# Optimization experiments

Measured on AMD Instinct MI355X. Metric: run time of the kernel, lower is better.

## Reference

```python
import jax, jax.numpy as jnp
import numpy as np
import math

B, T, E = 16, 4096, 1024
WIN = 15
EPS = 1e-6
HALF = T // 2


def _make_linear(key, out_f, in_f):
    k1, k2 = jax.random.split(key)
    lim = 1.0 / math.sqrt(in_f)
    W = jax.random.uniform(k1, (out_f, in_f), minval=-lim, maxval=lim, dtype=jnp.float32)
    b = jax.random.uniform(k2, (out_f,), minval=-lim, maxval=lim, dtype=jnp.float32)
    return W, b


def setup_inputs() -> dict:
    key = jax.random.key(0)
    ks = jax.random.split(key, 5)
    x = jax.random.normal(ks[0], (B, T, E), dtype=jnp.float32)
    taper = jnp.linspace(1.0, 0.0, T, dtype=jnp.float32)
    cW1, cb1 = _make_linear(ks[1], HALF, T)
    cW2, cb2 = _make_linear(ks[2], HALF, HALF)
    pW1, pb1 = _make_linear(ks[3], HALF, T)
    pW2, pb2 = _make_linear(ks[4], HALF, HALF)
    return {"x": x, "taper": taper,
            "cW1": cW1, "cb1": cb1, "cW2": cW2, "cb2": cb2,
            "pW1": pW1, "pb1": pb1, "pW2": pW2, "pb2": pb2}


def _compressor(h, W1, b1, W2, b2):
    # Linear -> SiLU -> Linear -> Tanh  (torch Linear: y = h @ W^T + b)
    h = jax.nn.silu(h @ W1.T + b1)
    return jnp.tanh(h @ W2.T + b2)


def _tdiff_raw(c0):
    Bb, Tt = c0.shape
    xp = jnp.pad(c0, ((0, 0), (WIN, 0)))  # left pad with zeros
    num = jnp.zeros_like(c0)
    for d in range(1, WIN + 1):  # small fixed loop over window lags
        num = num + float(d) * jax.lax.dynamic_slice_in_dim(xp, WIN - d, Tt, axis=1)
    i = jnp.arange(Tt, dtype=jnp.float32)
    s = jnp.minimum(i, float(WIN))
    norm = s * (s + 1.0) * 0.5
    return jnp.where(norm > 0, num / jnp.maximum(norm, 1.0), 0.0)


def reference(x, taper, cW1, cb1, cW2, cb2, pW1, pb1, pW2, pb2):
    x_t = x * taper[None, :, None]          # (B,T,E) tapered in time
    c0 = x_t[..., 0]                         # (B,T)
    r = jnp.abs(c0) + EPS
    start = jnp.where(c0 >= 0, 0.0, jnp.float32(math.pi))
    v = jnp.clip(x_t[..., 1:] / r[..., None], -1.0 + EPS, 1.0 - EPS)
    phases = start + jnp.arcsin(v).sum(axis=-1)  # (B,T)
    tdiff = _compressor(_tdiff_raw(c0), pW1, pb1, pW2, pb2)   # (B,T/2)
    thash = _compressor(phases, cW1, cb1, cW2, cb2)           # (B,T/2)
    return jnp.stack([thash, tdiff], axis=-1)                 # (B,T/2,2)
```

## Files before the change

### kernel.cpp

```cpp
#include <hip/hip_runtime.h>
#include <math.h>

#define BB 16
#define TT 4096
#define EE 1024
#define HALF 2048
#define WIN 15
#define EPSF 1e-6f
#define PI_F   3.14159265358979323846f
#define PIO2_F 1.57079632679489662f

__device__ __forceinline__ float asin_clamped(float t, float LO, float HI) {
    float c  = __builtin_amdgcn_fmed3f(t, LO, HI);
    float a  = fabsf(c);
    float z1 = c * c;
    float z2 = fmaf(a, -0.5f, 0.5f);
    bool big = a > 0.5f;
    float z  = big ? z2 : z1;
    float sq;
    asm("v_sqrt_f32 %0, %1" : "=v"(sq) : "v"(z2));
    float s  = big ? sq : a;
    float p = fmaf(z, 4.2163199048e-2f, 2.4181311049e-2f);
    p = fmaf(z, p, 4.5470025998e-2f);
    p = fmaf(z, p, 7.4953002686e-2f);
    p = fmaf(z, p, 1.6666752422e-1f);
    float r  = fmaf(s * z, p, s);
    float rb = fmaf(-2.0f, r, PIO2_F);
    r = big ? rb : r;
    return copysignf(r, c);
}

__global__ void phase_tdiff_kernel(const float* __restrict__ x,
                                   const float* __restrict__ taper,
                                   float* __restrict__ phases_b,
                                   float* __restrict__ tdiff_b) {
    const int wave = threadIdx.x >> 6;
    const int lane = threadIdx.x & 63;
    const int row  = blockIdx.x * 4 + wave;
    const int b = row >> 12;
    const int t = row & (TT - 1);
    const float tap = taper[t];
    const float* xr = x + (size_t)row * EE;

    float xd = 0.0f, tapd = 0.0f;
    const int td = t - lane;
    const bool do_d = (lane >= 1) && (lane <= WIN) && (lane <= t);
    if (do_d) {
        xd   = x[((size_t)b * TT + td) * EE];
        tapd = taper[td];
    }

    const float c0 = xr[0] * tap;
    const float r = fabsf(c0) + EPSF;
    const float scale = tap / r;
    const float start = (c0 >= 0.0f) ? 0.0f : PI_F;
    const float LO = -1.0f + EPSF, HI = 1.0f - EPSF;

    const float4* xr4 = (const float4*)xr;
    float sum = 0.0f;
    #pragma unroll
    for (int j = 0; j < 4; ++j) {
        float4 v = xr4[j * 64 + lane];
        float a0 = asin_clamped(v.x * scale, LO, HI);
        if ((j | lane) == 0) a0 = 0.0f;
        sum += a0;
        sum += asin_clamped(v.y * scale, LO, HI);
        sum += asin_clamped(v.z * scale, LO, HI);
        sum += asin_clamped(v.w * scale, LO, HI);
    }
    #pragma unroll
    for (int off = 32; off > 0; off >>= 1)
        sum += __shfl_xor(sum, off, 64);

    float contrib = do_d ? ((float)lane * xd * tapd) : 0.0f;
    #pragma unroll
    for (int off = 8; off > 0; off >>= 1)
        contrib += __shfl_xor(contrib, off, 64);

    if (lane == 0) {
        phases_b[b * TT + t] = start + sum;
        const int s = (t < WIN) ? t : WIN;
        const float norm = 0.5f * (float)s * (float)(s + 1);
        tdiff_b[b * TT + t] = (norm > 0.0f) ? (contrib / norm) : 0.0f;
    }
}

__device__ __forceinline__ void gld_lds16(const float* g, float* l) {
    __builtin_amdgcn_global_load_lds(
        (const __attribute__((address_space(1))) unsigned int*)g,
        (__attribute__((address_space(3))) unsigned int*)l,
        16, 0, 0);
}

template <int K, int MODE>
__global__ void __launch_bounds__(256)
gemm_kernel(const float* __restrict__ A0, const float* __restrict__ W0,
            const float* __restrict__ bias0, float* __restrict__ out0,
            const float* __restrict__ A1, const float* __restrict__ W1,
            const float* __restrict__ bias1, float* __restrict__ out1) {
    constexpr int KT = 512;
    constexpr int NT = K / KT;
    constexpr int LROW = KT + 4;
    __shared__ float als[2][16 * LROW];

    const int nb = HALF / 8;
    const int g = blockIdx.x / nb;
    const int obase = (blockIdx.x % nb) * 8;

    const float* A    = g ? A1 : A0;
    const float* W    = g ? W1 : W0;
    const float* bias = g ? bias1 : bias0;
    float* out        = g ? out1 : out0;

    const int wv   = threadIdx.x >> 6;
    const int lane = threadIdx.x & 63;
    const int col0 = obase + wv * 2;
    const int col1 = col0 + 1;
    const float* w0p = W + (size_t)col0 * K;
    const float* w1p = W + (size_t)col1 * K;

    auto stage = [&](int t, int s) {
        #pragma unroll
        for (int i = 0; i < 4; ++i) {
            const int br = wv * 4 + i;
            const float* src = A + (size_t)br * K + t * KT + lane * 4;
            float* dst = &als[s][br * LROW];
            gld_lds16(src, dst);
            gld_lds16(src + 256, dst + 256);
        }
    };

    float acc0[16], acc1[16];
    #pragma unroll
    for (int i = 0; i < 16; ++i) { acc0[i] = 0.0f; acc1[i] = 0.0f; }

    stage(0, 0);

    for (int t = 0; t < NT; ++t) {
        const int cur = t & 1;

        float4 w0v[2], w1v[2];
        #pragma unroll
        for (int s2 = 0; s2 < 2; ++s2) {
            w0v[s2] = *(const float4*)(w0p + t * KT + s2 * 256 + lane * 4);
            w1v[s2] = *(const float4*)(w1p + t * KT + s2 * 256 + lane * 4);
        }

        if (t + 1 < NT) {
            stage(t + 1, cur ^ 1);
            asm volatile("s_waitcnt vmcnt(8)" ::: "memory");
        } else {
            asm volatile("s_waitcnt vmcnt(0)" ::: "memory");
        }
        __builtin_amdgcn_s_barrier();
        __builtin_amdgcn_sched_barrier(0);

        #pragma unroll
        for (int s2 = 0; s2 < 2; ++s2) {
            #pragma unroll
            for (int br = 0; br < 16; ++br) {
                const float4 a4 = *(const float4*)&als[cur][br * LROW + s2 * 256 + lane * 4];
                acc0[br] += w0v[s2].x*a4.x + w0v[s2].y*a4.y + w0v[s2].z*a4.z + w0v[s2].w*a4.w;
                acc1[br] += w1v[s2].x*a4.x + w1v[s2].y*a4.y + w1v[s2].z*a4.z + w1v[s2].w*a4.w;
            }
        }
        __builtin_amdgcn_sched_barrier(0);
        __builtin_amdgcn_s_barrier();
    }

    #pragma unroll
    for (int off = 32; off > 0; off >>= 1) {
        #pragma unroll
        for (int i = 0; i < 16; ++i) {
            acc0[i] += __shfl_xor(acc0[i], off, 64);
            acc1[i] += __shfl_xor(acc1[i], off, 64);
        }
    }

    const bool isw0 = (lane == 0), isw1 = (lane == 32);
    if (isw0 || isw1) {
        const int o = isw0 ? col0 : col1;
        const float bs = bias[o];
        #pragma unroll
        for (int i = 0; i < 16; ++i) {
            float s = (isw0 ? acc0[i] : acc1[i]) + bs;
            if (MODE == 0) {
                s = s / (1.0f + expf(-s));
                out[(size_t)i * HALF + o] = s;
            } else {
                s = tanhf(s);
                out[(size_t)i * (HALF * 2) + o * 2 + g] = s;
            }
        }
    }
}

extern "C" void kernel_launch(void* const* d_in, const int* in_sizes, int n_in,
                              void* d_out, int out_size, void* d_ws, size_t ws_size,
                              hipStream_t stream) {
    const float* x     = (const float*)d_in[0];
    const float* taper = (const float*)d_in[1];
    const float* cW1   = (const float*)d_in[2];
    const float* cb1   = (const float*)d_in[3];
    const float* cW2   = (const float*)d_in[4];
    const float* cb2   = (const float*)d_in[5];
    const float* pW1   = (const float*)d_in[6];
    const float* pb1   = (const float*)d_in[7];
    const float* pW2   = (const float*)d_in[8];
    const float* pb2   = (const float*)d_in[9];
    float* out = (float*)d_out;
    float* ws  = (float*)d_ws;

    float* phases_b = ws;
    float* tdiff_b  = ws + 65536;
    float* H1_b     = ws + 131072;
    float* H2_b     = ws + 163840;

    phase_tdiff_kernel<<<BB * TT / 4, 256, 0, stream>>>(x, taper, phases_b, tdiff_b);
    gemm_kernel<TT, 0><<<512, 256, 0, stream>>>(phases_b, cW1, cb1, H1_b,
                                                tdiff_b, pW1, pb1, H2_b);
    gemm_kernel<HALF, 1><<<512, 256, 0, stream>>>(H1_b, cW2, cb2, out,
                                                  H2_b, pW2, pb2, out);
}
```

Baseline: 98.19 us.

## Prefetch GEMM weight registers one tile ahead with manual two-stage unroll

Restructures the GEMM K-loop into a two-tile unrolled body with ping-pong weight register sets. Each tile's W loads are issued alongside the next A stage, so global weight latency overlaps with compute on the current tile instead of being waited on at the start of each iteration. This needs more vector registers and waitcnt counts tuned by hand, and it assumes NT is even (it is for K=4096 and 2048).

Result: no change. 100.1 us (+1.9%).

```diff
diff --git a/kernel.cpp b/kernel.cpp
--- a/kernel.cpp
+++ b/kernel.cpp
@@ -130,43 +130,61 @@
         }
     };
 
+#define LOADW(W0R, W1R, T) do {                                           \
+        _Pragma("unroll")                                                 \
+        for (int s2 = 0; s2 < 2; ++s2) {                                  \
+            W0R[s2] = *(const float4*)(w0p + (T) * KT + s2 * 256 + lane * 4); \
+            W1R[s2] = *(const float4*)(w1p + (T) * KT + s2 * 256 + lane * 4); \
+        }                                                                 \
+    } while (0)
+
+#define COMPUTE(S, W0R, W1R) do {                                         \
+        _Pragma("unroll")                                                 \
+        for (int s2 = 0; s2 < 2; ++s2) {                                  \
+            _Pragma("unroll")                                             \
+            for (int br = 0; br < 16; ++br) {                             \
+                const float4 a4 = *(const float4*)&als[S][br * LROW + s2 * 256 + lane * 4]; \
+                acc0[br] += W0R[s2].x*a4.x + W0R[s2].y*a4.y + W0R[s2].z*a4.z + W0R[s2].w*a4.w; \
+                acc1[br] += W1R[s2].x*a4.x + W1R[s2].y*a4.y + W1R[s2].z*a4.z + W1R[s2].w*a4.w; \
+            }                                                             \
+        }                                                                 \
+    } while (0)
+
     float acc0[16], acc1[16];
     #pragma unroll
     for (int i = 0; i < 16; ++i) { acc0[i] = 0.0f; acc1[i] = 0.0f; }
 
+    float4 wA0[2], wA1[2], wB0[2], wB1[2];
     stage(0, 0);
-
-    for (int t = 0; t < NT; ++t) {
-        const int cur = t & 1;
-
-        float4 w0v[2], w1v[2];
-        #pragma unroll
-        for (int s2 = 0; s2 < 2; ++s2) {
-            w0v[s2] = *(const float4*)(w0p + t * KT + s2 * 256 + lane * 4);
-            w1v[s2] = *(const float4*)(w1p + t * KT + s2 * 256 + lane * 4);
-        }
-
-        if (t + 1 < NT) {
-            stage(t + 1, cur ^ 1);
-            asm volatile("s_waitcnt vmcnt(8)" ::: "memory");
+    LOADW(wA0, wA1, 0);
+
+    #pragma unroll 1
+    for (int t = 0; t < NT; t += 2) {
+        stage(t + 1, 1);
+        LOADW(wB0, wB1, t + 1);
+        asm volatile("s_waitcnt vmcnt(12)" ::: "memory");
+        __builtin_amdgcn_s_barrier();
+        __builtin_amdgcn_sched_barrier(0);
+        COMPUTE(0, wA0, wA1);
+        __builtin_amdgcn_sched_barrier(0);
+        __builtin_amdgcn_s_barrier();
+
+        if (t + 2 < NT) {
+            stage(t + 2, 0);
+            LOADW(wA0, wA1, t + 2);
+            asm volatile("s_waitcnt vmcnt(12)" ::: "memory");
         } else {
             asm volatile("s_waitcnt vmcnt(0)" ::: "memory");
         }
         __builtin_amdgcn_s_barrier();
         __builtin_amdgcn_sched_barrier(0);
-
-        #pragma unroll
-        for (int s2 = 0; s2 < 2; ++s2) {
-            #pragma unroll
-            for (int br = 0; br < 16; ++br) {
-                const float4 a4 = *(const float4*)&als[cur][br * LROW + s2 * 256 + lane * 4];
-                acc0[br] += w0v[s2].x*a4.x + w0v[s2].y*a4.y + w0v[s2].z*a4.z + w0v[s2].w*a4.w;
-                acc1[br] += w1v[s2].x*a4.x + w1v[s2].y*a4.y + w1v[s2].z*a4.z + w1v[s2].w*a4.w;
-            }
-        }
-        __builtin_amdgcn_sched_barrier(0);
-        __builtin_amdgcn_s_barrier();
-    }
+        COMPUTE(1, wB0, wB1);
+        __builtin_amdgcn_sched_barrier(0);
+        __builtin_amdgcn_s_barrier();
+    }
+
+#undef LOADW
+#undef COMPUTE
 
     #pragma unroll
     for (int off = 32; off > 0; off >>= 1) {
```

## Use 512-thread GEMM blocks with large single-buffered K chunks

Applied to the files above, without the earlier changes.

The GEMM kernel now runs 8 waves per block, each covering 16 output columns, on 256 blocks. It stages 2048-wide K chunks of the activation rows into LDS in one shot instead of double-buffered 512-wide tiles, and loads all weight float4s for the chunk into registers up front. This cuts the number of barriers and K iterations and shares each LDS-staged activation chunk across more output columns. In exchange it drops the prefetch overlap, uses about 131 KB of LDS per block, and raises register pressure with 16 float4 weight registers per thread, which could lower occupancy.

Result: slower. 207.8 us (+111.6%).

```diff
diff --git a/kernel.cpp b/kernel.cpp
--- a/kernel.cpp
+++ b/kernel.cpp
@@ -93,19 +93,19 @@
 }
 
 template <int K, int MODE>
-__global__ void __launch_bounds__(256)
+__global__ void __launch_bounds__(512)
 gemm_kernel(const float* __restrict__ A0, const float* __restrict__ W0,
             const float* __restrict__ bias0, float* __restrict__ out0,
             const float* __restrict__ A1, const float* __restrict__ W1,
             const float* __restrict__ bias1, float* __restrict__ out1) {
-    constexpr int KT = 512;
-    constexpr int NT = K / KT;
-    constexpr int LROW = KT + 4;
-    __shared__ float als[2][16 * LROW];
-
-    const int nb = HALF / 8;
+    constexpr int CK = 2048;
+    constexpr int NC = K / CK;
+    constexpr int LR = CK + 4;
+    __shared__ float als[16 * LR];
+
+    const int nb = HALF / 16;
     const int g = blockIdx.x / nb;
-    const int obase = (blockIdx.x % nb) * 8;
+    const int obase = (blockIdx.x % nb) * 16;
 
     const float* A    = g ? A1 : A0;
     const float* W    = g ? W1 : W0;
@@ -119,53 +119,42 @@
     const float* w0p = W + (size_t)col0 * K;
     const float* w1p = W + (size_t)col1 * K;
 
-    auto stage = [&](int t, int s) {
-        #pragma unroll
-        for (int i = 0; i < 4; ++i) {
-            const int br = wv * 4 + i;
-            const float* src = A + (size_t)br * K + t * KT + lane * 4;
-            float* dst = &als[s][br * LROW];
-            gld_lds16(src, dst);
-            gld_lds16(src + 256, dst + 256);
-        }
-    };
-
     float acc0[16], acc1[16];
     #pragma unroll
     for (int i = 0; i < 16; ++i) { acc0[i] = 0.0f; acc1[i] = 0.0f; }
 
-    stage(0, 0);
-
-    for (int t = 0; t < NT; ++t) {
-        const int cur = t & 1;
-
-        float4 w0v[2], w1v[2];
-        #pragma unroll
-        for (int s2 = 0; s2 < 2; ++s2) {
-            w0v[s2] = *(const float4*)(w0p + t * KT + s2 * 256 + lane * 4);
-            w1v[s2] = *(const float4*)(w1p + t * KT + s2 * 256 + lane * 4);
-        }
-
-        if (t + 1 < NT) {
-            stage(t + 1, cur ^ 1);
-            asm volatile("s_waitcnt vmcnt(8)" ::: "memory");
-        } else {
-            asm volatile("s_waitcnt vmcnt(0)" ::: "memory");
-        }
-        __builtin_amdgcn_s_barrier();
-        __builtin_amdgcn_sched_barrier(0);
-
-        #pragma unroll
-        for (int s2 = 0; s2 < 2; ++s2) {
+    #pragma unroll 1
+    for (int c = 0; c < NC; ++c) {
+        if (c > 0) __syncthreads();
+
+        #pragma unroll
+        for (int i = 0; i < 2; ++i) {
+            const int br = wv * 2 + i;
+            const float* src = A + (size_t)br * K + c * CK + lane * 4;
+            float* dst = &als[br * LR];
+            #pragma unroll
+            for (int s = 0; s < 8; ++s)
+                gld_lds16(src + s * 256, dst + s * 256);
+        }
+
+        float4 w0r[8], w1r[8];
+        #pragma unroll
+        for (int s = 0; s < 8; ++s) {
+            w0r[s] = *(const float4*)(w0p + c * CK + s * 256 + lane * 4);
+            w1r[s] = *(const float4*)(w1p + c * CK + s * 256 + lane * 4);
+        }
+
+        __syncthreads();
+
+        #pragma unroll
+        for (int s = 0; s < 8; ++s) {
             #pragma unroll
             for (int br = 0; br < 16; ++br) {
-                const float4 a4 = *(const float4*)&als[cur][br * LROW + s2 * 256 + lane * 4];
-                acc0[br] += w0v[s2].x*a4.x + w0v[s2].y*a4.y + w0v[s2].z*a4.z + w0v[s2].w*a4.w;
-                acc1[br] += w1v[s2].x*a4.x + w1v[s2].y*a4.y + w1v[s2].z*a4.z + w1v[s2].w*a4.w;
+                const float4 a4 = *(const float4*)&als[br * LR + s * 256 + lane * 4];
+                acc0[br] += w0r[s].x*a4.x + w0r[s].y*a4.y + w0r[s].z*a4.z + w0r[s].w*a4.w;
+                acc1[br] += w1r[s].x*a4.x + w1r[s].y*a4.y + w1r[s].z*a4.z + w1r[s].w*a4.w;
             }
         }
-        __builtin_amdgcn_sched_barrier(0);
-        __builtin_amdgcn_s_barrier();
     }
 
     #pragma unroll
@@ -217,8 +206,8 @@
     float* H2_b     = ws + 163840;
 
     phase_tdiff_kernel<<<BB * TT / 4, 256, 0, stream>>>(x, taper, phases_b, tdiff_b);
-    gemm_kernel<TT, 0><<<512, 256, 0, stream>>>(phases_b, cW1, cb1, H1_b,
+    gemm_kernel<TT, 0><<<256, 512, 0, stream>>>(phases_b, cW1, cb1, H1_b,
                                                 tdiff_b, pW1, pb1, H2_b);
-    gemm_kernel<HALF, 1><<<512, 256, 0, stream>>>(H1_b, cW2, cb2, out,
+    gemm_kernel<HALF, 1><<<256, 512, 0, stream>>>(H1_b, cW2, cb2, out,
                                                   H2_b, pW2, pb2, out);
 }
```
